# Kernel optimization log

Hardware: AMD Instinct MI355X
Metric: run time of the kernel (lower is better)

The kernel has to match this reference:

```python
import jax, jax.numpy as jnp
import numpy as np

N = 50000
E = 800000
IN, H, OUT = 128, 96, 64
BN_EPS = 1e-5


def setup_inputs() -> dict:
    key = jax.random.key(0)
    ks = jax.random.split(key, 16)
    x = jax.random.normal(ks[0], (N, IN), dtype=jnp.float32)
    edge_index = jax.random.randint(ks[1], (2, E), 0, N, dtype=jnp.int64)
    edge_weight = jax.random.uniform(ks[2], (E,), dtype=jnp.float32)
    def lin(k, fo, fi):
        # PyG glorot-ish init
        s = 1.0 / np.sqrt(fi)
        return jax.random.uniform(k, (fo, fi), minval=-s, maxval=s, dtype=jnp.float32)
    W1, b1 = lin(ks[3], H, IN), jnp.zeros((H,), jnp.float32)
    W2, b2 = lin(ks[4], H, H), jnp.zeros((H,), jnp.float32)
    W3, b3 = lin(ks[5], OUT, H), jnp.zeros((OUT,), jnp.float32)
    g1 = jnp.ones((H,), jnp.float32); beta1 = jnp.zeros((H,), jnp.float32)
    m1 = 0.1 * jax.random.normal(ks[6], (H,), dtype=jnp.float32)
    v1 = jnp.abs(1.0 + 0.1 * jax.random.normal(ks[7], (H,), dtype=jnp.float32))
    g2 = jnp.ones((H,), jnp.float32); beta2 = jnp.zeros((H,), jnp.float32)
    m2 = 0.1 * jax.random.normal(ks[8], (H,), dtype=jnp.float32)
    v2 = jnp.abs(1.0 + 0.1 * jax.random.normal(ks[9], (H,), dtype=jnp.float32))
    return dict(x=x, edge_index=edge_index, edge_weight=edge_weight,
                W1=W1, b1=b1, W2=W2, b2=b2, W3=W3, b3=b3,
                g1=g1, beta1=beta1, m1=m1, v1=v1,
                g2=g2, beta2=beta2, m2=m2, v2=v2)


def gcn_norm(edge_index, edge_weight, n):
    # PyG gcn_norm with add_self_loops=True, fill_value=1.0
    loop = jnp.arange(n, dtype=edge_index.dtype)
    row = jnp.concatenate([edge_index[0], loop])  # sources
    col = jnp.concatenate([edge_index[1], loop])  # targets
    ew = jnp.concatenate([edge_weight, jnp.ones((n,), edge_weight.dtype)])
    deg = jax.ops.segment_sum(ew, col, num_segments=n)
    dis = jnp.where(deg > 0, jax.lax.rsqrt(deg), 0.0)  # inf -> 0 masked_fill
    norm = dis[row] * ew * dis[col]
    return row, col, norm


def gcn_conv(x, row, col, norm, W, b, n):
    xw = x @ W.T                       # [N, F_out] dense transform first
    msg = norm[:, None] * xw[row]      # [E+N, F_out] gather + edge scale
    out = jax.ops.segment_sum(msg, col, num_segments=n)  # scatter-add
    return out + b


def bn_eval(x, gamma, beta, mean, var):
    return (x - mean) * jax.lax.rsqrt(var + BN_EPS) * gamma + beta


def reference(x, edge_index, edge_weight, W1, b1, W2, b2, W3, b3,
              g1, beta1, m1, v1, g2, beta2, m2, v2):
    n = x.shape[0]
    row, col, norm = gcn_norm(edge_index, edge_weight, n)  # cached=True: shared
    h = gcn_conv(x, row, col, norm, W1, b1, n)
    h = jax.nn.relu(bn_eval(h, g1, beta1, m1, v1))
    h = gcn_conv(h, row, col, norm, W2, b2, n)
    h = jax.nn.relu(bn_eval(h, g2, beta2, m2, v2))
    out = gcn_conv(h, row, col, norm, W3, b3, n)
    return out
```

## Files before the change

kernel.cpp:

```cpp
#include <hip/hip_runtime.h>
#include <hip/hip_fp16.h>


constexpr float BN_EPS = 1e-5f;
constexpr float DEG_SCALE = 131072.0f;
constexpr float INV_DEG_SCALE = 1.0f / 131072.0f;
constexpr float NORM_SCALE = 32768.0f;
constexpr float INV_NORM_SCALE = 1.0f / 32768.0f;

typedef _Float16 f16x8 __attribute__((ext_vector_type(8)));
typedef float f32x4 __attribute__((ext_vector_type(4)));


template <int K, int F, bool F32X, bool F32W>
__device__ __forceinline__ void gemm_block(const void* __restrict__ Xin,
                                           const void* __restrict__ Win,
                                           _Float16* __restrict__ Y,
                                           int n0b, int tid, int n,
                                           _Float16* lds) {
    constexpr int KT = K / 32;
    constexpr int FT = F / 16;
    constexpr int LROW = (F == 96) ? 104 : 72;
    int wave = tid >> 6;
    int lane = tid & 63;
    int quad = lane >> 4;
    int r = lane & 15;
    int n0 = n0b + wave * 16;
    bool active = (n0 < n);

    if (active) {
        f16x8 a[KT];
        if (F32X) {
            const float* xr = (const float*)Xin + (size_t)(n0 + r) * K + quad * 8;
#pragma unroll
            for (int kt = 0; kt < KT; ++kt) {
                float4 v0 = *(const float4*)(xr + kt * 32);
                float4 v1 = *(const float4*)(xr + kt * 32 + 4);
                f16x8 t = {(_Float16)v0.x, (_Float16)v0.y, (_Float16)v0.z, (_Float16)v0.w,
                           (_Float16)v1.x, (_Float16)v1.y, (_Float16)v1.z, (_Float16)v1.w};
                a[kt] = t;
            }
        } else {
            const f16x8* xr = (const f16x8*)((const _Float16*)Xin + (size_t)(n0 + r) * K + quad * 8);
#pragma unroll
            for (int kt = 0; kt < KT; ++kt) a[kt] = xr[kt * 4];
        }

        f32x4 acc[FT];
#pragma unroll
        for (int ft = 0; ft < FT; ++ft) acc[ft] = (f32x4){0.f, 0.f, 0.f, 0.f};

#pragma unroll
        for (int kt = 0; kt < KT; ++kt) {
#pragma unroll
            for (int ft = 0; ft < FT; ++ft) {
                f16x8 b;
                if (F32W) {
                    const float* wr = (const float*)Win + (size_t)(ft * 16 + r) * K + kt * 32 + quad * 8;
                    float4 v0 = *(const float4*)wr;
                    float4 v1 = *(const float4*)(wr + 4);
                    f16x8 t = {(_Float16)v0.x, (_Float16)v0.y, (_Float16)v0.z, (_Float16)v0.w,
                               (_Float16)v1.x, (_Float16)v1.y, (_Float16)v1.z, (_Float16)v1.w};
                    b = t;
                } else {
                    b = *(const f16x8*)((const _Float16*)Win + (size_t)(ft * 16 + r) * K + kt * 32 + quad * 8);
                }
                acc[ft] = __builtin_amdgcn_mfma_f32_16x16x32_f16(a[kt], b, acc[ft], 0, 0, 0);
            }
        }

#pragma unroll
        for (int ft = 0; ft < FT; ++ft) {
#pragma unroll
            for (int reg = 0; reg < 4; ++reg) {
                int lr = wave * 16 + quad * 4 + reg;
                lds[(size_t)lr * LROW + ft * 16 + r] = (_Float16)acc[ft][reg];
            }
        }
    }
    __syncthreads();

    constexpr int CPR = F / 8;
    constexpr int TOTAL = 64 * CPR;
    for (int i = tid; i < TOTAL; i += 256) {
        int row = i / CPR, c = i - row * CPR;
        int grow = n0b + row;
        if (grow < n)
            *(uint4*)(Y + (size_t)grow * F + c * 8) =
                *(const uint4*)(lds + (size_t)row * LROW + c * 8);
    }
}

template <int K, int F>
__global__ __launch_bounds__(256) void k_gemm(const _Float16* __restrict__ X,
                                              const _Float16* __restrict__ Wh,
                                              _Float16* __restrict__ Y, int n) {
    __shared__ _Float16 lds[64 * 104];
    gemm_block<K, F, false, false>(X, Wh, Y, blockIdx.x * 64, threadIdx.x, n, lds);
}


__global__ __launch_bounds__(256) void k_mega(
    const int* __restrict__ col_idx, const float* __restrict__ ew,
    unsigned* packed, unsigned char* rank, int e_cnt, int pair_b,
    const float* __restrict__ x, const float* __restrict__ W1,
    _Float16* __restrict__ bufA, int n,
    const float* __restrict__ W2, const float* __restrict__ W3,
    _Float16* __restrict__ w2h, _Float16* __restrict__ w3h,
    int w2n4, int w3n4) {
    __shared__ _Float16 lds[64 * 104];
    int b = blockIdx.x;
    if (b < 2 * pair_b) {
        int q = b >> 1;
        if ((b & 1) == 0) {
#pragma unroll
            for (int j = 0; j < 4; ++j) {
                int e = q * 1024 + j * 256 + (int)threadIdx.x;
                if (e < e_cnt) {
                    int c = col_idx[e];
                    unsigned wfix = (unsigned)(ew[e] * DEG_SCALE + 0.5f);
                    unsigned old = atomicAdd(&packed[c], 0x1000000u | wfix);
                    rank[e] = (unsigned char)(old >> 24);
                }
            }
        } else {
            gemm_block<128, 96, true, true>(x, W1, bufA, q * 64, threadIdx.x, n, lds);
        }
    } else {
        int i = (b - 2 * pair_b) * 256 + (int)threadIdx.x;
        const float* src; _Float16* dst; int o;
        if (i < w2n4) { src = W2; dst = w2h; o = i; }
        else if (i < w2n4 + w3n4) { src = W3; dst = w3h; o = i - w2n4; }
        else return;
        float4 v = ((const float4*)src)[o];
        __half2 h0 = __floats2half2_rn(v.x, v.y);
        __half2 h1 = __floats2half2_rn(v.z, v.w);
        *(uint2*)(dst + (size_t)o * 4) = make_uint2(*(unsigned*)&h0, *(unsigned*)&h1);
    }
}


__global__ void k_scan1(const unsigned* __restrict__ packed,
                        int* bsum, float* dis, int n) {
    __shared__ int s[256];
    int i = blockIdx.x * 256 + threadIdx.x;
    int cnt = 0;
    if (i < n) {
        unsigned p = packed[i];
        cnt = (int)(p >> 24);
        float wsum = (float)(p & 0xFFFFFFu) * INV_DEG_SCALE;
        dis[i] = rsqrtf(1.0f + wsum);
    }
    s[threadIdx.x] = cnt;
    __syncthreads();
    for (int off = 128; off > 0; off >>= 1) {
        if ((int)threadIdx.x < off) s[threadIdx.x] += s[threadIdx.x + off];
        __syncthreads();
    }
    if (threadIdx.x == 0) bsum[blockIdx.x] = s[0];
}

__global__ void k_scan23(const unsigned* __restrict__ packed,
                         const int* __restrict__ bsum,
                         int* row_ptr, int n, int e_total, int nb) {
    __shared__ int sb[256];
    __shared__ int s[256];
    int t = threadIdx.x;
    int bv = (t < nb) ? bsum[t] : 0;
    sb[t] = bv;
    __syncthreads();
    for (int off = 1; off < 256; off <<= 1) {
        int x = (t >= off) ? sb[t - off] : 0;
        __syncthreads();
        sb[t] += x;
        __syncthreads();
    }
    int boff = (blockIdx.x == 0) ? 0 : sb[blockIdx.x - 1];

    int i = blockIdx.x * 256 + t;
    int v = (i < n) ? (int)(packed[i] >> 24) : 0;
    s[t] = v;
    __syncthreads();
    for (int off = 1; off < 256; off <<= 1) {
        int x = (t >= off) ? s[t - off] : 0;
        __syncthreads();
        s[t] += x;
        __syncthreads();
    }
    int ex = s[t] - v + boff;
    if (i < n) row_ptr[i] = ex;
    if (i == 0) row_ptr[n] = e_total;
}

__global__ void k_fill(const int* __restrict__ row_idx, const int* __restrict__ col_idx,
                       const float* __restrict__ ew, const float* __restrict__ dis,
                       const int* __restrict__ row_ptr, const unsigned char* __restrict__ rank,
                       unsigned* ep, int e_cnt) {
    int e = blockIdx.x * 256 + threadIdx.x;
    if (e < e_cnt) {
        int r = row_idx[e];
        int c = col_idx[e];
        float nm = dis[r] * ew[e] * dis[c];
        unsigned q = (unsigned)(nm * NORM_SCALE + 0.5f);
        if (q > 65535u) q = 65535u;
        ep[row_ptr[c] + (int)rank[e]] = ((unsigned)r << 16) | q;
    }
}


__device__ inline void cvt8(uint4 u, float* f) {
    float2 t;
    t = __half22float2(*(const __half2*)&u.x); f[0] = t.x; f[1] = t.y;
    t = __half22float2(*(const __half2*)&u.y); f[2] = t.x; f[3] = t.y;
    t = __half22float2(*(const __half2*)&u.z); f[4] = t.x; f[5] = t.y;
    t = __half22float2(*(const __half2*)&u.w); f[6] = t.x; f[7] = t.y;
}

__device__ inline void h8_acc(uint4 u, float w, float acc[8]) {
    float2 a = __half22float2(*(const __half2*)&u.x);
    float2 b = __half22float2(*(const __half2*)&u.y);
    float2 c = __half22float2(*(const __half2*)&u.z);
    float2 d = __half22float2(*(const __half2*)&u.w);
    acc[0] = fmaf(w, a.x, acc[0]); acc[1] = fmaf(w, a.y, acc[1]);
    acc[2] = fmaf(w, b.x, acc[2]); acc[3] = fmaf(w, b.y, acc[3]);
    acc[4] = fmaf(w, c.x, acc[4]); acc[5] = fmaf(w, c.y, acc[5]);
    acc[6] = fmaf(w, d.x, acc[6]); acc[7] = fmaf(w, d.y, acc[7]);
}

template <int F, bool BN, bool F32OUT, int UNR>
__global__ __launch_bounds__(256) void k_aggr(
    const _Float16* __restrict__ xw, const int* __restrict__ row_ptr,
    const unsigned* __restrict__ ep,
    const float* __restrict__ dis, const float* __restrict__ bias,
    const float* __restrict__ g, const float* __restrict__ beta,
    const float* __restrict__ m, const float* __restrict__ v,
    void* __restrict__ out, int n) {
    constexpr int FQ = F / 8;
    int tg = blockIdx.x * 256 + threadIdx.x;
    int node = tg / FQ;
    int q = tg - node * FQ;
    if (node >= n) return;

    const uint4* __restrict__ base = (const uint4*)xw;

    float acc[8];
    {
        float d = dis[node];
        float d2 = d * d;
        uint4 sv = base[(size_t)node * FQ + q];
        float t[8];
        cvt8(sv, t);
#pragma unroll
        for (int j = 0; j < 8; ++j) acc[j] = d2 * t[j];
    }

    int e0 = row_ptr[node], e1 = row_ptr[node + 1];
    int e = e0;
    if (UNR == 8) {
        for (; e + 8 <= e1; e += 8) {
            unsigned p0 = ep[e + 0], p1 = ep[e + 1], p2 = ep[e + 2], p3 = ep[e + 3];
            unsigned p4 = ep[e + 4], p5 = ep[e + 5], p6 = ep[e + 6], p7 = ep[e + 7];
            uint4 x0 = base[(size_t)(p0 >> 16) * FQ + q];
            uint4 x1 = base[(size_t)(p1 >> 16) * FQ + q];
            uint4 x2 = base[(size_t)(p2 >> 16) * FQ + q];
            uint4 x3 = base[(size_t)(p3 >> 16) * FQ + q];
            uint4 x4 = base[(size_t)(p4 >> 16) * FQ + q];
            uint4 x5 = base[(size_t)(p5 >> 16) * FQ + q];
            uint4 x6 = base[(size_t)(p6 >> 16) * FQ + q];
            uint4 x7 = base[(size_t)(p7 >> 16) * FQ + q];
            h8_acc(x0, (float)(p0 & 0xffffu) * INV_NORM_SCALE, acc);
            h8_acc(x1, (float)(p1 & 0xffffu) * INV_NORM_SCALE, acc);
            h8_acc(x2, (float)(p2 & 0xffffu) * INV_NORM_SCALE, acc);
            h8_acc(x3, (float)(p3 & 0xffffu) * INV_NORM_SCALE, acc);
            h8_acc(x4, (float)(p4 & 0xffffu) * INV_NORM_SCALE, acc);
            h8_acc(x5, (float)(p5 & 0xffffu) * INV_NORM_SCALE, acc);
            h8_acc(x6, (float)(p6 & 0xffffu) * INV_NORM_SCALE, acc);
            h8_acc(x7, (float)(p7 & 0xffffu) * INV_NORM_SCALE, acc);
        }
    }
    for (; e + 4 <= e1; e += 4) {
        unsigned p0 = ep[e + 0], p1 = ep[e + 1], p2 = ep[e + 2], p3 = ep[e + 3];
        uint4 x0 = base[(size_t)(p0 >> 16) * FQ + q];
        uint4 x1 = base[(size_t)(p1 >> 16) * FQ + q];
        uint4 x2 = base[(size_t)(p2 >> 16) * FQ + q];
        uint4 x3 = base[(size_t)(p3 >> 16) * FQ + q];
        h8_acc(x0, (float)(p0 & 0xffffu) * INV_NORM_SCALE, acc);
        h8_acc(x1, (float)(p1 & 0xffffu) * INV_NORM_SCALE, acc);
        h8_acc(x2, (float)(p2 & 0xffffu) * INV_NORM_SCALE, acc);
        h8_acc(x3, (float)(p3 & 0xffffu) * INV_NORM_SCALE, acc);
    }
    for (; e < e1; ++e) {
        unsigned p = ep[e];
        uint4 xv = base[(size_t)(p >> 16) * FQ + q];
        h8_acc(xv, (float)(p & 0xffffu) * INV_NORM_SCALE, acc);
    }

    int fb = q * 8;
    const float4* bb = (const float4*)(bias + fb);
    float4 b0 = bb[0], b1 = bb[1];
    acc[0] += b0.x; acc[1] += b0.y; acc[2] += b0.z; acc[3] += b0.w;
    acc[4] += b1.x; acc[5] += b1.y; acc[6] += b1.z; acc[7] += b1.w;
    if (BN) {
#pragma unroll
        for (int j = 0; j < 8; ++j) {
            acc[j] = fmaxf((acc[j] - m[fb + j]) * rsqrtf(v[fb + j] + BN_EPS) * g[fb + j]
                           + beta[fb + j], 0.f);
        }
    }
    if (F32OUT) {
        float* op = (float*)out + (size_t)node * F + fb;
        *(float4*)(op + 0) = make_float4(acc[0], acc[1], acc[2], acc[3]);
        *(float4*)(op + 4) = make_float4(acc[4], acc[5], acc[6], acc[7]);
    } else {
        __half2 h0 = __floats2half2_rn(acc[0], acc[1]);
        __half2 h1 = __floats2half2_rn(acc[2], acc[3]);
        __half2 h2 = __floats2half2_rn(acc[4], acc[5]);
        __half2 h3 = __floats2half2_rn(acc[6], acc[7]);
        uint4 u = make_uint4(*(unsigned*)&h0, *(unsigned*)&h1,
                             *(unsigned*)&h2, *(unsigned*)&h3);
        ((uint4*)out)[(size_t)node * FQ + q] = u;
    }
}


extern "C" void kernel_launch(void* const* d_in, const int* in_sizes, int n_in,
                              void* d_out, int out_size, void* d_ws, size_t ws_size,
                              hipStream_t stream) {
    constexpr int IN = 128, H = 96, OUT = 64;

    const float* x   = (const float*)d_in[0];
    const int*   ei  = (const int*)d_in[1];
    const float* ew  = (const float*)d_in[2];
    const float* W1  = (const float*)d_in[3];
    const float* b1  = (const float*)d_in[4];
    const float* W2  = (const float*)d_in[5];
    const float* b2  = (const float*)d_in[6];
    const float* W3  = (const float*)d_in[7];
    const float* b3  = (const float*)d_in[8];
    const float* g1  = (const float*)d_in[9];
    const float* be1 = (const float*)d_in[10];
    const float* m1  = (const float*)d_in[11];
    const float* v1  = (const float*)d_in[12];
    const float* g2  = (const float*)d_in[13];
    const float* be2 = (const float*)d_in[14];
    const float* m2  = (const float*)d_in[15];
    const float* v2  = (const float*)d_in[16];

    const int N = in_sizes[0] / IN;
    const int E = in_sizes[2];
    const int* row_idx = ei;
    const int* col_idx = ei + E;

    char* ws = (char*)d_ws;
    size_t off = 0;
    auto alloc = [&](size_t bytes) -> void* {
        void* p = ws + off;
        off = (off + bytes + 255) & ~(size_t)255;
        return p;
    };
    unsigned*  packed  = (unsigned*)alloc((size_t)N * 4);
    float*     dis     = (float*)alloc((size_t)N * 4);
    int*       row_ptr = (int*)alloc((size_t)(N + 1) * 4);
    int*       bsum    = (int*)alloc(256 * 4);
    unsigned char* rank = (unsigned char*)alloc((size_t)E);
    unsigned*  ep      = (unsigned*)alloc((size_t)E * 4);
    _Float16*  w2h     = (_Float16*)alloc((size_t)H * H * 2);
    _Float16*  w3h     = (_Float16*)alloc((size_t)OUT * H * 2);
    _Float16*  bufA    = (_Float16*)alloc((size_t)N * H * 2);
    _Float16*  bufB    = (_Float16*)alloc((size_t)N * H * 2);
    (void)ws_size; (void)n_in; (void)out_size;

    constexpr int W2N4 = H * H / 4, W3N4 = OUT * H / 4;
    const int NB = (N + 255) / 256;
    const int DEG1024 = (E + 1023) / 1024;
    const int GG = (N + 63) / 64;
    const int PAIR = (DEG1024 > GG) ? DEG1024 : GG;
    const int CVT_B = (W2N4 + W3N4 + 255) / 256;

    hipMemsetAsync(packed, 0, (size_t)N * 4, stream);
    k_mega<<<2 * PAIR + CVT_B, 256, 0, stream>>>(
        col_idx, ew, packed, rank, E, PAIR,
        x, W1, bufA, N, W2, W3, w2h, w3h, W2N4, W3N4);
    k_scan1<<<NB, 256, 0, stream>>>(packed, bsum, dis, N);
    k_scan23<<<NB, 256, 0, stream>>>(packed, bsum, row_ptr, N, E, NB);
    k_fill<<<(E + 255) / 256, 256, 0, stream>>>(row_idx, col_idx, ew, dis,
                                                row_ptr, rank, ep, E);

    const int GA96 = ((size_t)N * (H / 8) + 255) / 256;
    const int GA64 = ((size_t)N * (OUT / 8) + 255) / 256;

    k_aggr<H, true, false, 8><<<GA96, 256, 0, stream>>>(
        bufA, row_ptr, ep, dis, b1, g1, be1, m1, v1, bufB, N);

    k_gemm<H, H><<<GG, 256, 0, stream>>>(bufB, w2h, bufA, N);
    k_aggr<H, true, false, 4><<<GA96, 256, 0, stream>>>(
        bufA, row_ptr, ep, dis, b2, g2, be2, m2, v2, bufB, N);

    k_gemm<H, OUT><<<GG, 256, 0, stream>>>(bufB, w3h, bufA, N);
    k_aggr<OUT, false, true, 8><<<GA64, 256, 0, stream>>>(
        bufA, row_ptr, ep, dis, b3, nullptr, nullptr, nullptr, nullptr, d_out, N);
}
```

Baseline: 267.2 us.

## Sort nodes by degree via counting sort to balance aggregation wavefronts

Builds a degree histogram in k_scan1, scans it in descending order, and places node ids into a permutation so aggregation threads process nodes grouped by in-degree. Each k_aggr thread reads perm to pick its node, so lanes in a wavefront see similar loop trip counts and diverge less. The second aggregation also switches from 4-way to 8-way unrolling. The cost is two extra small kernels, extra atomics, and one more indirection per thread, and output writes for a wavefront now land on scattered nodes rather than contiguous ones.

Measured after the change: 271.6 us. Within noise of the previous version (+1.7%).

```diff
diff --git a/kernel.cpp b/kernel.cpp
--- a/kernel.cpp
+++ b/kernel.cpp
@@ -141,9 +141,12 @@
 
 
 __global__ void k_scan1(const unsigned* __restrict__ packed,
-                        int* bsum, float* dis, int n) {
+                        int* bsum, float* dis, unsigned* ghist, int n) {
     __shared__ int s[256];
-    int i = blockIdx.x * 256 + threadIdx.x;
+    __shared__ unsigned h[256];
+    int t = threadIdx.x;
+    h[t] = 0;
+    int i = blockIdx.x * 256 + t;
     int cnt = 0;
     if (i < n) {
         unsigned p = packed[i];
@@ -151,13 +154,50 @@
         float wsum = (float)(p & 0xFFFFFFu) * INV_DEG_SCALE;
         dis[i] = rsqrtf(1.0f + wsum);
     }
-    s[threadIdx.x] = cnt;
-    __syncthreads();
+    s[t] = cnt;
+    __syncthreads();
+    if (i < n) atomicAdd(&h[cnt], 1u);
     for (int off = 128; off > 0; off >>= 1) {
-        if ((int)threadIdx.x < off) s[threadIdx.x] += s[threadIdx.x + off];
-        __syncthreads();
-    }
-    if (threadIdx.x == 0) bsum[blockIdx.x] = s[0];
+        if (t < off) s[t] += s[t + off];
+        __syncthreads();
+    }
+    if (t == 0) bsum[blockIdx.x] = s[0];
+    if (h[t]) atomicAdd(&ghist[t], h[t]);
+}
+
+__global__ void k_binscan(const unsigned* __restrict__ ghist, unsigned* gstart) {
+    __shared__ unsigned sb[256];
+    int t = threadIdx.x;
+    unsigned v0 = ghist[255 - t];
+    sb[t] = v0;
+    __syncthreads();
+    for (int off = 1; off < 256; off <<= 1) {
+        unsigned x = (t >= off) ? sb[t - off] : 0;
+        __syncthreads();
+        sb[t] += x;
+        __syncthreads();
+    }
+    gstart[255 - t] = sb[t] - v0;
+}
+
+__global__ void k_place(const unsigned* __restrict__ packed,
+                        const unsigned* __restrict__ gstart,
+                        unsigned* gcur, int* perm, int n) {
+    __shared__ unsigned h[256];
+    __shared__ unsigned bbase[256];
+    int t = threadIdx.x;
+    h[t] = 0;
+    __syncthreads();
+    int i = blockIdx.x * 256 + t;
+    int k = 0; unsigned lrank = 0;
+    if (i < n) {
+        k = (int)(packed[i] >> 24);
+        lrank = atomicAdd(&h[k], 1u);
+    }
+    __syncthreads();
+    if (h[t]) bbase[t] = atomicAdd(&gcur[t], h[t]);
+    __syncthreads();
+    if (i < n) perm[gstart[k] + bbase[k] + lrank] = i;
 }
 
 __global__ void k_scan23(const unsigned* __restrict__ packed,
@@ -227,19 +267,20 @@
     acc[6] = fmaf(w, d.x, acc[6]); acc[7] = fmaf(w, d.y, acc[7]);
 }
 
-template <int F, bool BN, bool F32OUT, int UNR>
+template <int F, bool BN, bool F32OUT>
 __global__ __launch_bounds__(256) void k_aggr(
     const _Float16* __restrict__ xw, const int* __restrict__ row_ptr,
-    const unsigned* __restrict__ ep,
+    const unsigned* __restrict__ ep, const int* __restrict__ perm,
     const float* __restrict__ dis, const float* __restrict__ bias,
     const float* __restrict__ g, const float* __restrict__ beta,
     const float* __restrict__ m, const float* __restrict__ v,
     void* __restrict__ out, int n) {
     constexpr int FQ = F / 8;
     int tg = blockIdx.x * 256 + threadIdx.x;
-    int node = tg / FQ;
-    int q = tg - node * FQ;
-    if (node >= n) return;
+    int np = tg / FQ;
+    int q = tg - np * FQ;
+    if (np >= n) return;
+    int node = perm[np];
 
     const uint4* __restrict__ base = (const uint4*)xw;
 
@@ -256,27 +297,25 @@
 
     int e0 = row_ptr[node], e1 = row_ptr[node + 1];
     int e = e0;
-    if (UNR == 8) {
-        for (; e + 8 <= e1; e += 8) {
-            unsigned p0 = ep[e + 0], p1 = ep[e + 1], p2 = ep[e + 2], p3 = ep[e + 3];
-            unsigned p4 = ep[e + 4], p5 = ep[e + 5], p6 = ep[e + 6], p7 = ep[e + 7];
-            uint4 x0 = base[(size_t)(p0 >> 16) * FQ + q];
-            uint4 x1 = base[(size_t)(p1 >> 16) * FQ + q];
-            uint4 x2 = base[(size_t)(p2 >> 16) * FQ + q];
-            uint4 x3 = base[(size_t)(p3 >> 16) * FQ + q];
-            uint4 x4 = base[(size_t)(p4 >> 16) * FQ + q];
-            uint4 x5 = base[(size_t)(p5 >> 16) * FQ + q];
-            uint4 x6 = base[(size_t)(p6 >> 16) * FQ + q];
-            uint4 x7 = base[(size_t)(p7 >> 16) * FQ + q];
-            h8_acc(x0, (float)(p0 & 0xffffu) * INV_NORM_SCALE, acc);
-            h8_acc(x1, (float)(p1 & 0xffffu) * INV_NORM_SCALE, acc);
-            h8_acc(x2, (float)(p2 & 0xffffu) * INV_NORM_SCALE, acc);
-            h8_acc(x3, (float)(p3 & 0xffffu) * INV_NORM_SCALE, acc);
-            h8_acc(x4, (float)(p4 & 0xffffu) * INV_NORM_SCALE, acc);
-            h8_acc(x5, (float)(p5 & 0xffffu) * INV_NORM_SCALE, acc);
-            h8_acc(x6, (float)(p6 & 0xffffu) * INV_NORM_SCALE, acc);
-            h8_acc(x7, (float)(p7 & 0xffffu) * INV_NORM_SCALE, acc);
-        }
+    for (; e + 8 <= e1; e += 8) {
+        unsigned p0 = ep[e + 0], p1 = ep[e + 1], p2 = ep[e + 2], p3 = ep[e + 3];
+        unsigned p4 = ep[e + 4], p5 = ep[e + 5], p6 = ep[e + 6], p7 = ep[e + 7];
+        uint4 x0 = base[(size_t)(p0 >> 16) * FQ + q];
+        uint4 x1 = base[(size_t)(p1 >> 16) * FQ + q];
+        uint4 x2 = base[(size_t)(p2 >> 16) * FQ + q];
+        uint4 x3 = base[(size_t)(p3 >> 16) * FQ + q];
+        uint4 x4 = base[(size_t)(p4 >> 16) * FQ + q];
+        uint4 x5 = base[(size_t)(p5 >> 16) * FQ + q];
+        uint4 x6 = base[(size_t)(p6 >> 16) * FQ + q];
+        uint4 x7 = base[(size_t)(p7 >> 16) * FQ + q];
+        h8_acc(x0, (float)(p0 & 0xffffu) * INV_NORM_SCALE, acc);
+        h8_acc(x1, (float)(p1 & 0xffffu) * INV_NORM_SCALE, acc);
+        h8_acc(x2, (float)(p2 & 0xffffu) * INV_NORM_SCALE, acc);
+        h8_acc(x3, (float)(p3 & 0xffffu) * INV_NORM_SCALE, acc);
+        h8_acc(x4, (float)(p4 & 0xffffu) * INV_NORM_SCALE, acc);
+        h8_acc(x5, (float)(p5 & 0xffffu) * INV_NORM_SCALE, acc);
+        h8_acc(x6, (float)(p6 & 0xffffu) * INV_NORM_SCALE, acc);
+        h8_acc(x7, (float)(p7 & 0xffffu) * INV_NORM_SCALE, acc);
     }
     for (; e + 4 <= e1; e += 4) {
         unsigned p0 = ep[e + 0], p1 = ep[e + 1], p2 = ep[e + 2], p3 = ep[e + 3];
@@ -359,6 +398,11 @@
         return p;
     };
     unsigned*  packed  = (unsigned*)alloc((size_t)N * 4);
+    unsigned*  ghist   = (unsigned*)alloc(256 * 4);
+    unsigned*  gcur    = (unsigned*)alloc(256 * 4);
+    size_t zero_len = off;
+    unsigned*  gstart  = (unsigned*)alloc(256 * 4);
+    int*       perm    = (int*)alloc((size_t)N * 4);
     float*     dis     = (float*)alloc((size_t)N * 4);
     int*       row_ptr = (int*)alloc((size_t)(N + 1) * 4);
     int*       bsum    = (int*)alloc(256 * 4);
@@ -377,26 +421,28 @@
     const int PAIR = (DEG1024 > GG) ? DEG1024 : GG;
     const int CVT_B = (W2N4 + W3N4 + 255) / 256;
 
-    hipMemsetAsync(packed, 0, (size_t)N * 4, stream);
+    hipMemsetAsync(packed, 0, zero_len, stream);
     k_mega<<<2 * PAIR + CVT_B, 256, 0, stream>>>(
         col_idx, ew, packed, rank, E, PAIR,
         x, W1, bufA, N, W2, W3, w2h, w3h, W2N4, W3N4);
-    k_scan1<<<NB, 256, 0, stream>>>(packed, bsum, dis, N);
+    k_scan1<<<NB, 256, 0, stream>>>(packed, bsum, dis, ghist, N);
+    k_binscan<<<1, 256, 0, stream>>>(ghist, gstart);
     k_scan23<<<NB, 256, 0, stream>>>(packed, bsum, row_ptr, N, E, NB);
     k_fill<<<(E + 255) / 256, 256, 0, stream>>>(row_idx, col_idx, ew, dis,
                                                 row_ptr, rank, ep, E);
+    k_place<<<NB, 256, 0, stream>>>(packed, gstart, gcur, perm, N);
 
     const int GA96 = ((size_t)N * (H / 8) + 255) / 256;
     const int GA64 = ((size_t)N * (OUT / 8) + 255) / 256;
 
-    k_aggr<H, true, false, 8><<<GA96, 256, 0, stream>>>(
-        bufA, row_ptr, ep, dis, b1, g1, be1, m1, v1, bufB, N);
+    k_aggr<H, true, false><<<GA96, 256, 0, stream>>>(
+        bufA, row_ptr, ep, perm, dis, b1, g1, be1, m1, v1, bufB, N);
 
     k_gemm<H, H><<<GG, 256, 0, stream>>>(bufB, w2h, bufA, N);
-    k_aggr<H, true, false, 4><<<GA96, 256, 0, stream>>>(
-        bufA, row_ptr, ep, dis, b2, g2, be2, m2, v2, bufB, N);
+    k_aggr<H, true, false><<<GA96, 256, 0, stream>>>(
+        bufA, row_ptr, ep, perm, dis, b2, g2, be2, m2, v2, bufB, N);
 
     k_gemm<H, OUT><<<GG, 256, 0, stream>>>(bufB, w3h, bufA, N);
-    k_aggr<OUT, false, true, 8><<<GA64, 256, 0, stream>>>(
-        bufA, row_ptr, ep, dis, b3, nullptr, nullptr, nullptr, nullptr, d_out, N);
-}
+    k_aggr<OUT, false, true><<<GA64, 256, 0, stream>>>(
+        bufA, row_ptr, ep, perm, dis, b3, nullptr, nullptr, nullptr, nullptr, d_out, N);
+}
```

## Sort CSR edges by source-range buckets and factor target norm out of aggregation

Applied to the files above, without the earlier changes.

The degree atomic becomes a 64-bit packed counter with three per-bucket 10-bit counts keyed by source-node third, so edges within each target's CSR segment are grouped by source range. This is meant to improve locality of the gathered feature rows in the aggregation kernels. The target-side dis factor is also moved out of the per-edge norm and applied once per node, and the aggregation uses the 8-way unroll in all three layers. The cost is 64-bit atomics, a wider packed array, and an extra packed read in the fill kernel. The 10-bit count fields overflow silently if any target has 1024 or more in-edges from one bucket.

Result: faster. 258.3 us (-3.3%).

```diff
diff --git a/kernel.cpp b/kernel.cpp
--- a/kernel.cpp
+++ b/kernel.cpp
@@ -101,8 +101,10 @@
 
 
 __global__ __launch_bounds__(256) void k_mega(
-    const int* __restrict__ col_idx, const float* __restrict__ ew,
-    unsigned* packed, unsigned char* rank, int e_cnt, int pair_b,
+    const int* __restrict__ row_idx, const int* __restrict__ col_idx,
+    const float* __restrict__ ew,
+    unsigned long long* packed, unsigned char* rank, int e_cnt, int pair_b,
+    int t1, int t2,
     const float* __restrict__ x, const float* __restrict__ W1,
     _Float16* __restrict__ bufA, int n,
     const float* __restrict__ W2, const float* __restrict__ W3,
@@ -118,9 +120,13 @@
                 int e = q * 1024 + j * 256 + (int)threadIdx.x;
                 if (e < e_cnt) {
                     int c = col_idx[e];
+                    int r = row_idx[e];
+                    int t = (r >= t2) ? 2 : ((r >= t1) ? 1 : 0);
+                    int sh = 24 + 10 * t;
                     unsigned wfix = (unsigned)(ew[e] * DEG_SCALE + 0.5f);
-                    unsigned old = atomicAdd(&packed[c], 0x1000000u | wfix);
-                    rank[e] = (unsigned char)(old >> 24);
+                    unsigned long long inc = (1ull << sh) | (unsigned long long)wfix;
+                    unsigned long long old = atomicAdd(&packed[c], inc);
+                    rank[e] = (unsigned char)((old >> sh) & 0x3FFull);
                 }
             }
         } else {
@@ -140,15 +146,19 @@
 }
 
 
-__global__ void k_scan1(const unsigned* __restrict__ packed,
+__device__ __forceinline__ int pk_cnt(unsigned long long p) {
+    return (int)((p >> 24) & 0x3FF) + (int)((p >> 34) & 0x3FF) + (int)((p >> 44) & 0x3FF);
+}
+
+__global__ void k_scan1(const unsigned long long* __restrict__ packed,
                         int* bsum, float* dis, int n) {
     __shared__ int s[256];
     int i = blockIdx.x * 256 + threadIdx.x;
     int cnt = 0;
     if (i < n) {
-        unsigned p = packed[i];
-        cnt = (int)(p >> 24);
-        float wsum = (float)(p & 0xFFFFFFu) * INV_DEG_SCALE;
+        unsigned long long p = packed[i];
+        cnt = pk_cnt(p);
+        float wsum = (float)(unsigned)(p & 0xFFFFFFull) * INV_DEG_SCALE;
         dis[i] = rsqrtf(1.0f + wsum);
     }
     s[threadIdx.x] = cnt;
@@ -160,7 +170,7 @@
     if (threadIdx.x == 0) bsum[blockIdx.x] = s[0];
 }
 
-__global__ void k_scan23(const unsigned* __restrict__ packed,
+__global__ void k_scan23(const unsigned long long* __restrict__ packed,
                          const int* __restrict__ bsum,
                          int* row_ptr, int n, int e_total, int nb) {
     __shared__ int sb[256];
@@ -178,7 +188,7 @@
     int boff = (blockIdx.x == 0) ? 0 : sb[blockIdx.x - 1];
 
     int i = blockIdx.x * 256 + t;
-    int v = (i < n) ? (int)(packed[i] >> 24) : 0;
+    int v = (i < n) ? pk_cnt(packed[i]) : 0;
     s[t] = v;
     __syncthreads();
     for (int off = 1; off < 256; off <<= 1) {
@@ -195,15 +205,21 @@
 __global__ void k_fill(const int* __restrict__ row_idx, const int* __restrict__ col_idx,
                        const float* __restrict__ ew, const float* __restrict__ dis,
                        const int* __restrict__ row_ptr, const unsigned char* __restrict__ rank,
-                       unsigned* ep, int e_cnt) {
+                       const unsigned long long* __restrict__ packed,
+                       unsigned* ep, int e_cnt, int t1, int t2) {
     int e = blockIdx.x * 256 + threadIdx.x;
     if (e < e_cnt) {
         int r = row_idx[e];
         int c = col_idx[e];
-        float nm = dis[r] * ew[e] * dis[c];
+        unsigned long long p = packed[c];
+        int c0 = (int)((p >> 24) & 0x3FF);
+        int c1 = (int)((p >> 34) & 0x3FF);
+        int t = (r >= t2) ? 2 : ((r >= t1) ? 1 : 0);
+        int off = (t > 0 ? c0 : 0) + (t > 1 ? c1 : 0);
+        float nm = dis[r] * ew[e];
         unsigned q = (unsigned)(nm * NORM_SCALE + 0.5f);
         if (q > 65535u) q = 65535u;
-        ep[row_ptr[c] + (int)rank[e]] = ((unsigned)r << 16) | q;
+        ep[row_ptr[c] + off + (int)rank[e]] = ((unsigned)r << 16) | q;
     }
 }
 
@@ -227,7 +243,7 @@
     acc[6] = fmaf(w, d.x, acc[6]); acc[7] = fmaf(w, d.y, acc[7]);
 }
 
-template <int F, bool BN, bool F32OUT, int UNR>
+template <int F, bool BN, bool F32OUT>
 __global__ __launch_bounds__(256) void k_aggr(
     const _Float16* __restrict__ xw, const int* __restrict__ row_ptr,
     const unsigned* __restrict__ ep,
@@ -243,40 +259,37 @@
 
     const uint4* __restrict__ base = (const uint4*)xw;
 
+    float d = dis[node];
     float acc[8];
     {
-        float d = dis[node];
-        float d2 = d * d;
         uint4 sv = base[(size_t)node * FQ + q];
         float t[8];
         cvt8(sv, t);
 #pragma unroll
-        for (int j = 0; j < 8; ++j) acc[j] = d2 * t[j];
+        for (int j = 0; j < 8; ++j) acc[j] = d * t[j];
     }
 
     int e0 = row_ptr[node], e1 = row_ptr[node + 1];
     int e = e0;
-    if (UNR == 8) {
-        for (; e + 8 <= e1; e += 8) {
-            unsigned p0 = ep[e + 0], p1 = ep[e + 1], p2 = ep[e + 2], p3 = ep[e + 3];
-            unsigned p4 = ep[e + 4], p5 = ep[e + 5], p6 = ep[e + 6], p7 = ep[e + 7];
-            uint4 x0 = base[(size_t)(p0 >> 16) * FQ + q];
-            uint4 x1 = base[(size_t)(p1 >> 16) * FQ + q];
-            uint4 x2 = base[(size_t)(p2 >> 16) * FQ + q];
-            uint4 x3 = base[(size_t)(p3 >> 16) * FQ + q];
-            uint4 x4 = base[(size_t)(p4 >> 16) * FQ + q];
-            uint4 x5 = base[(size_t)(p5 >> 16) * FQ + q];
-            uint4 x6 = base[(size_t)(p6 >> 16) * FQ + q];
-            uint4 x7 = base[(size_t)(p7 >> 16) * FQ + q];
-            h8_acc(x0, (float)(p0 & 0xffffu) * INV_NORM_SCALE, acc);
-            h8_acc(x1, (float)(p1 & 0xffffu) * INV_NORM_SCALE, acc);
-            h8_acc(x2, (float)(p2 & 0xffffu) * INV_NORM_SCALE, acc);
-            h8_acc(x3, (float)(p3 & 0xffffu) * INV_NORM_SCALE, acc);
-            h8_acc(x4, (float)(p4 & 0xffffu) * INV_NORM_SCALE, acc);
-            h8_acc(x5, (float)(p5 & 0xffffu) * INV_NORM_SCALE, acc);
-            h8_acc(x6, (float)(p6 & 0xffffu) * INV_NORM_SCALE, acc);
-            h8_acc(x7, (float)(p7 & 0xffffu) * INV_NORM_SCALE, acc);
-        }
+    for (; e + 8 <= e1; e += 8) {
+        unsigned p0 = ep[e + 0], p1 = ep[e + 1], p2 = ep[e + 2], p3 = ep[e + 3];
+        unsigned p4 = ep[e + 4], p5 = ep[e + 5], p6 = ep[e + 6], p7 = ep[e + 7];
+        uint4 x0 = base[(size_t)(p0 >> 16) * FQ + q];
+        uint4 x1 = base[(size_t)(p1 >> 16) * FQ + q];
+        uint4 x2 = base[(size_t)(p2 >> 16) * FQ + q];
+        uint4 x3 = base[(size_t)(p3 >> 16) * FQ + q];
+        uint4 x4 = base[(size_t)(p4 >> 16) * FQ + q];
+        uint4 x5 = base[(size_t)(p5 >> 16) * FQ + q];
+        uint4 x6 = base[(size_t)(p6 >> 16) * FQ + q];
+        uint4 x7 = base[(size_t)(p7 >> 16) * FQ + q];
+        h8_acc(x0, (float)(p0 & 0xffffu) * INV_NORM_SCALE, acc);
+        h8_acc(x1, (float)(p1 & 0xffffu) * INV_NORM_SCALE, acc);
+        h8_acc(x2, (float)(p2 & 0xffffu) * INV_NORM_SCALE, acc);
+        h8_acc(x3, (float)(p3 & 0xffffu) * INV_NORM_SCALE, acc);
+        h8_acc(x4, (float)(p4 & 0xffffu) * INV_NORM_SCALE, acc);
+        h8_acc(x5, (float)(p5 & 0xffffu) * INV_NORM_SCALE, acc);
+        h8_acc(x6, (float)(p6 & 0xffffu) * INV_NORM_SCALE, acc);
+        h8_acc(x7, (float)(p7 & 0xffffu) * INV_NORM_SCALE, acc);
     }
     for (; e + 4 <= e1; e += 4) {
         unsigned p0 = ep[e + 0], p1 = ep[e + 1], p2 = ep[e + 2], p3 = ep[e + 3];
@@ -298,8 +311,10 @@
     int fb = q * 8;
     const float4* bb = (const float4*)(bias + fb);
     float4 b0 = bb[0], b1 = bb[1];
-    acc[0] += b0.x; acc[1] += b0.y; acc[2] += b0.z; acc[3] += b0.w;
-    acc[4] += b1.x; acc[5] += b1.y; acc[6] += b1.z; acc[7] += b1.w;
+    acc[0] = fmaf(acc[0], d, b0.x); acc[1] = fmaf(acc[1], d, b0.y);
+    acc[2] = fmaf(acc[2], d, b0.z); acc[3] = fmaf(acc[3], d, b0.w);
+    acc[4] = fmaf(acc[4], d, b1.x); acc[5] = fmaf(acc[5], d, b1.y);
+    acc[6] = fmaf(acc[6], d, b1.z); acc[7] = fmaf(acc[7], d, b1.w);
     if (BN) {
 #pragma unroll
         for (int j = 0; j < 8; ++j) {
@@ -350,6 +365,7 @@
     const int E = in_sizes[2];
     const int* row_idx = ei;
     const int* col_idx = ei + E;
+    const int T1 = N / 3, T2 = 2 * (N / 3);
 
     char* ws = (char*)d_ws;
     size_t off = 0;
@@ -358,7 +374,7 @@
         off = (off + bytes + 255) & ~(size_t)255;
         return p;
     };
-    unsigned*  packed  = (unsigned*)alloc((size_t)N * 4);
+    unsigned long long* packed = (unsigned long long*)alloc((size_t)N * 8);
     float*     dis     = (float*)alloc((size_t)N * 4);
     int*       row_ptr = (int*)alloc((size_t)(N + 1) * 4);
     int*       bsum    = (int*)alloc(256 * 4);
@@ -377,26 +393,26 @@
     const int PAIR = (DEG1024 > GG) ? DEG1024 : GG;
     const int CVT_B = (W2N4 + W3N4 + 255) / 256;
 
-    hipMemsetAsync(packed, 0, (size_t)N * 4, stream);
+    hipMemsetAsync(packed, 0, (size_t)N * 8, stream);
     k_mega<<<2 * PAIR + CVT_B, 256, 0, stream>>>(
-        col_idx, ew, packed, rank, E, PAIR,
+        row_idx, col_idx, ew, packed, rank, E, PAIR, T1, T2,
         x, W1, bufA, N, W2, W3, w2h, w3h, W2N4, W3N4);
     k_scan1<<<NB, 256, 0, stream>>>(packed, bsum, dis, N);
     k_scan23<<<NB, 256, 0, stream>>>(packed, bsum, row_ptr, N, E, NB);
     k_fill<<<(E + 255) / 256, 256, 0, stream>>>(row_idx, col_idx, ew, dis,
-                                                row_ptr, rank, ep, E);
+                                                row_ptr, rank, packed, ep, E, T1, T2);
 
     const int GA96 = ((size_t)N * (H / 8) + 255) / 256;
     const int GA64 = ((size_t)N * (OUT / 8) + 255) / 256;
 
-    k_aggr<H, true, false, 8><<<GA96, 256, 0, stream>>>(
+    k_aggr<H, true, false><<<GA96, 256, 0, stream>>>(
         bufA, row_ptr, ep, dis, b1, g1, be1, m1, v1, bufB, N);
 
     k_gemm<H, H><<<GG, 256, 0, stream>>>(bufB, w2h, bufA, N);
-    k_aggr<H, true, false, 4><<<GA96, 256, 0, stream>>>(
+    k_aggr<H, true, false><<<GA96, 256, 0, stream>>>(
         bufA, row_ptr, ep, dis, b2, g2, be2, m2, v2, bufB, N);
 
     k_gemm<H, OUT><<<GG, 256, 0, stream>>>(bufB, w3h, bufA, N);
-    k_aggr<OUT, false, true, 8><<<GA64, 256, 0, stream>>>(
+    k_aggr<OUT, false, true><<<GA64, 256, 0, stream>>>(
         bufA, row_ptr, ep, dis, b3, nullptr, nullptr, nullptr, nullptr, d_out, N);
 }
```
